# Optimization experiments

Hardware: AMD Instinct MI355X
Metric: run time of the kernel (lower is better)

Reference implementation:

```python
import jax, jax.numpy as jnp
import numpy as np

N = 50000       # node_num
E_RND = 1600000 # random edges (avg degree 32)
IN = 256        # in_dim
OUT = 128       # out_dim
NB = 10000      # queried nodes batch
SLOPE = 0.1     # leaky_relu slope_ratio


def setup_inputs() -> dict:
    key = jax.random.key(0)
    k = jax.random.split(key, 6)
    feats = jax.random.normal(k[0], (N, IN), dtype=jnp.float32)
    W = jax.random.normal(k[1], (OUT, IN), dtype=jnp.float32) * 0.05
    b = jax.random.normal(k[2], (OUT,), dtype=jnp.float32) * 0.05
    a = jax.random.normal(k[3], (2 * OUT,), dtype=jnp.float32) * 0.05
    rnd = jax.random.randint(k[4], (E_RND, 2), 0, N)
    loops = jnp.stack([jnp.arange(N), jnp.arange(N)], axis=1)  # self-loops, as in torch code
    edges = jnp.concatenate([rnd, loops], axis=0).astype(jnp.int32)  # [E,2] = (dst, src)
    node_idx = jax.random.randint(k[5], (NB,), 0, N).astype(jnp.int32)
    return dict(feats=feats, W=W, b=b, a=a, edges=edges, node_idx=node_idx)


def reference(feats, W, b, a, edges, node_idx):
    n = feats.shape[0]
    emb = feats @ W.T + b                      # [N, OUT]  (out_linear_layer)
    out_dim = emb.shape[1]
    # concat(emb[dst], emb[src]) @ a  ==  (emb @ a1)[dst] + (emb @ a2)[src]
    s_dst = emb @ a[:out_dim]                  # [N]
    s_src = emb @ a[out_dim:]                  # [N]
    dst, src = edges[:, 0], edges[:, 1]
    score = jnp.exp(jax.nn.leaky_relu(s_dst[dst] + s_src[src], negative_slope=SLOPE))  # [E]
    # sparse.mm(matrix, emb) and sparse.mm(matrix, ones) as segment sums over dst
    num = jax.ops.segment_sum(score[:, None] * emb[src], dst, num_segments=n)  # [N, OUT]
    den = jax.ops.segment_sum(score, dst, num_segments=n)                       # [N]
    out = num / den[:, None]
    return out[node_idx]
```

## Files before the change

kernel.cpp:

```cpp
#include <hip/hip_runtime.h>

#define IN_DIM 256
#define OUT_DIM 128
#define SLOPE 0.1f
#define CAP 128

typedef short bf16x8 __attribute__((ext_vector_type(8)));
typedef float f32x4  __attribute__((ext_vector_type(4)));
typedef unsigned short ushort4v __attribute__((ext_vector_type(4)));

__device__ __forceinline__ unsigned short f2bf(float f) {
    unsigned u = __builtin_bit_cast(unsigned, f);
    return (unsigned short)((u + 0x7FFFu + ((u >> 16) & 1u)) >> 16);
}

__device__ __forceinline__ void gld_lds16(const void* g, void* l) {
    __builtin_amdgcn_global_load_lds(
        (const __attribute__((address_space(1))) void*)g,
        (__attribute__((address_space(3))) void*)l, 16, 0, 0);
}

__global__ __launch_bounds__(256) void cvt_kernel(
    const float* __restrict__ feats, const float* __restrict__ W,
    unsigned short* __restrict__ fb, unsigned short* __restrict__ wb,
    int nf4, int nw4)
{
    const int stride = gridDim.x * blockDim.x;
    const int total = nf4 + nw4;
    for (int i = blockIdx.x * blockDim.x + threadIdx.x; i < total; i += stride) {
        float4 v;
        if (i < nf4) v = reinterpret_cast<const float4*>(feats)[i];
        else         v = reinterpret_cast<const float4*>(W)[i - nf4];
        ushort4v o;
        o[0] = f2bf(v.x); o[1] = f2bf(v.y); o[2] = f2bf(v.z); o[3] = f2bf(v.w);
        if (i < nf4) *reinterpret_cast<ushort4v*>(&fb[4 * (size_t)i]) = o;
        else         *reinterpret_cast<ushort4v*>(&wb[4 * (size_t)(i - nf4)]) = o;
    }
}

__global__ __launch_bounds__(256) void gemm_mfma_kernel(
    const unsigned short* __restrict__ fb, const unsigned short* __restrict__ wb,
    const float* __restrict__ bias, const float* __restrict__ a,
    unsigned short* __restrict__ emb_bf, float* __restrict__ s_dst,
    float* __restrict__ s_src, int* __restrict__ needed,
    int* __restrict__ cur, int n)
{
    __shared__ __align__(16) unsigned short A_s[128 * 128];
    __shared__ __align__(16) unsigned short W_s[128 * 128];
    __shared__ float sd_l[2][128];
    __shared__ float ss_l[2][128];

    const int t    = threadIdx.x;
    const int lane = t & 63;
    const int wid  = t >> 6;
    const int wr   = wid >> 1;
    const int wc   = wid & 1;
    const int row0 = blockIdx.x * 128;

    if (t < 128) {
        const int ci = row0 + t;
        if (ci < n) { needed[ci] = 0; cur[ci] = 0; }
    }

    const int rlo = lane >> 4;
    const int cA  = lane & 15;

    const f32x4 z4 = {0.f, 0.f, 0.f, 0.f};
    f32x4 acc[4][4];
    #pragma unroll
    for (int mi = 0; mi < 4; ++mi)
        #pragma unroll
        for (int ni = 0; ni < 4; ++ni) acc[mi][ni] = z4;

    for (int ph = 0; ph < 2; ++ph) {
        const int k0 = ph * 128;
        if (ph) __syncthreads();

        #pragma unroll
        for (int j = 0; j < 8; ++j) {
            const int slot = wid * 8 + j;
            const int r    = slot * 4 + rlo;
            const int ch   = cA ^ (r & 7);
            gld_lds16(fb + (size_t)(row0 + r) * IN_DIM + k0 + (ch << 3),
                      &A_s[slot * 512]);
            gld_lds16(wb + (size_t)r * IN_DIM + k0 + (ch << 3),
                      &W_s[slot * 512]);
        }
        __syncthreads();

        #pragma unroll
        for (int ks = 0; ks < 4; ++ks) {
            const int kf = ks * 32 + (lane >> 4) * 8;
            bf16x8 af[4], wf[4];
            #pragma unroll
            for (int mi = 0; mi < 4; ++mi) {
                const int row = wr * 64 + mi * 16 + (lane & 15);
                const int off = (row * 128 + kf) ^ ((row & 7) << 3);
                af[mi] = *(const bf16x8*)&A_s[off];
            }
            #pragma unroll
            for (int ni = 0; ni < 4; ++ni) {
                const int col = wc * 64 + ni * 16 + (lane & 15);
                const int off = (col * 128 + kf) ^ ((col & 7) << 3);
                wf[ni] = *(const bf16x8*)&W_s[off];
            }
            #pragma unroll
            for (int mi = 0; mi < 4; ++mi)
                #pragma unroll
                for (int ni = 0; ni < 4; ++ni)
                    acc[mi][ni] = __builtin_amdgcn_mfma_f32_16x16x32_bf16(
                        af[mi], wf[ni], acc[mi][ni], 0, 0, 0);
        }
    }

    float bcol[4], avd[4], avs[4];
    #pragma unroll
    for (int ni = 0; ni < 4; ++ni) {
        const int col = wc * 64 + ni * 16 + (lane & 15);
        bcol[ni] = bias[col];
        avd[ni]  = a[col];
        avs[ni]  = a[OUT_DIM + col];
    }

    #pragma unroll
    for (int mi = 0; mi < 4; ++mi) {
        #pragma unroll
        for (int j = 0; j < 4; ++j) {
            const int rib = wr * 64 + mi * 16 + (lane >> 4) * 4 + j;
            const int row = row0 + rib;
            float pd = 0.f, ps = 0.f;
            if (row < n) {
                #pragma unroll
                for (int ni = 0; ni < 4; ++ni) {
                    const float v = acc[mi][ni][j] + bcol[ni];
                    emb_bf[(size_t)row * OUT_DIM + wc * 64 + ni * 16 + (lane & 15)] = f2bf(v);
                    pd = fmaf(v, avd[ni], pd);
                    ps = fmaf(v, avs[ni], ps);
                }
            }
            pd += __shfl_xor(pd, 1); ps += __shfl_xor(ps, 1);
            pd += __shfl_xor(pd, 2); ps += __shfl_xor(ps, 2);
            pd += __shfl_xor(pd, 4); ps += __shfl_xor(ps, 4);
            pd += __shfl_xor(pd, 8); ps += __shfl_xor(ps, 8);
            if ((lane & 15) == 0) { sd_l[wc][rib] = pd; ss_l[wc][rib] = ps; }
        }
    }
    __syncthreads();
    if (t < 128) {
        const int row = row0 + t;
        if (row < n) {
            s_dst[row] = sd_l[0][t] + sd_l[1][t];
            s_src[row] = ss_l[0][t] + ss_l[1][t];
        }
    }
}

__global__ void flag_kernel(const int* __restrict__ node_idx,
                            int* __restrict__ needed, int nb)
{
    const int i = blockIdx.x * blockDim.x + threadIdx.x;
    if (i < nb) needed[node_idx[i]] = 1;
}

__global__ __launch_bounds__(256) void scatter_kernel(
    const int* __restrict__ edges, const int* __restrict__ needed,
    int* __restrict__ cur, const float* __restrict__ s_dst,
    const float* __restrict__ s_src, int2* __restrict__ ew, int E)
{
    const int e = blockIdx.x * blockDim.x + threadIdx.x;
    if (e >= E) return;
    const int2 ed = reinterpret_cast<const int2*>(edges)[e];
    if (needed[ed.x]) {
        const float x = s_dst[ed.x] + s_src[ed.y];
        const float w = __expf(x >= 0.f ? x : SLOPE * x);
        const int p = atomicAdd(&cur[ed.x], 1);
        if (p < CAP)
            ew[(size_t)ed.x * CAP + p] = make_int2(ed.y, __float_as_int(w));
    }
}

__global__ __launch_bounds__(256) void agg_out_kernel(
    const int* __restrict__ node_idx, const int* __restrict__ cur,
    const int2* __restrict__ ew, const unsigned short* __restrict__ emb_bf,
    float* __restrict__ out, int nb)
{
    const int w    = (int)((blockIdx.x * blockDim.x + threadIdx.x) >> 6);
    const int lane = threadIdx.x & 63;
    if (w >= nb) return;

    const int dst = node_idx[w];
    int m = cur[dst];
    if (m > CAP) m = CAP;
    const int2* __restrict__ bucket = ew + (size_t)dst * CAP;

    float accx = 0.f, accy = 0.f, den = 0.f;

    for (int base = 0; base < m; base += 64) {
        const int rem = min(64, m - base);
        int   src = 0;
        float wt  = 0.f;
        if (lane < rem) {
            const int2 q = bucket[base + lane];
            src = q.x;
            wt  = __int_as_float(q.y);
        }
        int i = 0;
        for (; i + 4 <= rem; i += 4) {
            const int   s0 = __shfl(src, i),     s1 = __shfl(src, i + 1);
            const int   s2 = __shfl(src, i + 2), s3 = __shfl(src, i + 3);
            const float w0 = __shfl(wt, i),      w1 = __shfl(wt, i + 1);
            const float w2 = __shfl(wt, i + 2),  w3 = __shfl(wt, i + 3);
            const unsigned b0 = *(const unsigned*)&emb_bf[(size_t)s0 * OUT_DIM + 2 * lane];
            const unsigned b1 = *(const unsigned*)&emb_bf[(size_t)s1 * OUT_DIM + 2 * lane];
            const unsigned b2 = *(const unsigned*)&emb_bf[(size_t)s2 * OUT_DIM + 2 * lane];
            const unsigned b3 = *(const unsigned*)&emb_bf[(size_t)s3 * OUT_DIM + 2 * lane];
            den += (w0 + w1) + (w2 + w3);
            accx = fmaf(w0, __int_as_float((int)(b0 << 16)), accx);
            accy = fmaf(w0, __int_as_float((int)(b0 & 0xFFFF0000u)), accy);
            accx = fmaf(w1, __int_as_float((int)(b1 << 16)), accx);
            accy = fmaf(w1, __int_as_float((int)(b1 & 0xFFFF0000u)), accy);
            accx = fmaf(w2, __int_as_float((int)(b2 << 16)), accx);
            accy = fmaf(w2, __int_as_float((int)(b2 & 0xFFFF0000u)), accy);
            accx = fmaf(w3, __int_as_float((int)(b3 << 16)), accx);
            accy = fmaf(w3, __int_as_float((int)(b3 & 0xFFFF0000u)), accy);
        }
        for (; i < rem; ++i) {
            const int   s0 = __shfl(src, i);
            const float w0 = __shfl(wt, i);
            const unsigned b0 = *(const unsigned*)&emb_bf[(size_t)s0 * OUT_DIM + 2 * lane];
            den += w0;
            accx = fmaf(w0, __int_as_float((int)(b0 << 16)), accx);
            accy = fmaf(w0, __int_as_float((int)(b0 & 0xFFFF0000u)), accy);
        }
    }

    const float inv = 1.0f / den;
    float2 o; o.x = accx * inv; o.y = accy * inv;
    *reinterpret_cast<float2*>(&out[(size_t)w * OUT_DIM + 2 * lane]) = o;
}

extern "C" void kernel_launch(void* const* d_in, const int* in_sizes, int n_in,
                              void* d_out, int out_size, void* d_ws, size_t ws_size,
                              hipStream_t stream)
{
    const float* feats    = (const float*)d_in[0];
    const float* W        = (const float*)d_in[1];
    const float* bias     = (const float*)d_in[2];
    const float* a        = (const float*)d_in[3];
    const int*   edges    = (const int*)d_in[4];
    const int*   node_idx = (const int*)d_in[5];
    float*       out      = (float*)d_out;

    const int n  = in_sizes[0] / IN_DIM;
    const int E  = in_sizes[4] / 2;
    const int nb = in_sizes[5];
    const int npad = ((n + 127) / 128) * 128;

    char* ws = (char*)d_ws;
    unsigned short* emb_bf = (unsigned short*)ws;
    ws += (size_t)n * OUT_DIM * sizeof(unsigned short);
    unsigned short* fb = (unsigned short*)ws;
    ws += (size_t)npad * IN_DIM * sizeof(unsigned short);
    unsigned short* wb = (unsigned short*)ws;
    ws += (size_t)OUT_DIM * IN_DIM * sizeof(unsigned short);
    float* s_dst = (float*)ws;  ws += (size_t)(n + 4) * sizeof(float);
    float* s_src = (float*)ws;  ws += (size_t)(n + 4) * sizeof(float);
    int*   needed= (int*)ws;    ws += (size_t)(n + 4) * sizeof(int);
    int*   cur   = (int*)ws;    ws += (size_t)(n + 4) * sizeof(int);
    int2*  ew    = (int2*)ws;   ws += (size_t)n * CAP * sizeof(int2);

    const int nf4 = n * IN_DIM / 4;
    const int nw4 = OUT_DIM * IN_DIM / 4;

    cvt_kernel      <<<2048, 256, 0, stream>>>(feats, W, fb, wb, nf4, nw4);
    gemm_mfma_kernel<<<npad / 128, 256, 0, stream>>>(
        fb, wb, bias, a, emb_bf, s_dst, s_src, needed, cur, n);
    flag_kernel     <<<(nb + 255) / 256, 256, 0, stream>>>(node_idx, needed, nb);
    scatter_kernel  <<<(E + 255) / 256, 256, 0, stream>>>(edges, needed, cur, s_dst, s_src, ew, E);
    agg_out_kernel  <<<(nb + 3) / 4, 256, 0, stream>>>(node_idx, cur, ew, emb_bf, out, nb);
}
```

Measured before the change: 69.12 us.

## Compute attention scores from fp32 feats via folded W^T a vectors before GEMM

```diff
diff --git a/kernel.cpp b/kernel.cpp
--- a/kernel.cpp
+++ b/kernel.cpp
@@ -20,55 +20,119 @@
         (__attribute__((address_space(3))) void*)l, 16, 0, 0);
 }
 
-__global__ __launch_bounds__(256) void cvt_kernel(
-    const float* __restrict__ feats, const float* __restrict__ W,
-    unsigned short* __restrict__ fb, unsigned short* __restrict__ wb,
-    int nf4, int nw4)
-{
-    const int stride = gridDim.x * blockDim.x;
-    const int total = nf4 + nw4;
-    for (int i = blockIdx.x * blockDim.x + threadIdx.x; i < total; i += stride) {
-        float4 v;
-        if (i < nf4) v = reinterpret_cast<const float4*>(feats)[i];
-        else         v = reinterpret_cast<const float4*>(W)[i - nf4];
+__global__ __launch_bounds__(256) void uv_kernel(
+    const float* __restrict__ W, const float* __restrict__ a,
+    const float* __restrict__ bias, float* __restrict__ uv)
+{
+    const int k = threadIdx.x;
+    float u = 0.f, v = 0.f;
+    for (int j = 0; j < OUT_DIM; ++j) {
+        const float w = W[(size_t)j * IN_DIM + k];
+        u = fmaf(a[j], w, u);
+        v = fmaf(a[OUT_DIM + j], w, v);
+    }
+    uv[k] = u;
+    uv[256 + k] = v;
+    if (k == 0) {
+        float cd = 0.f, cs = 0.f;
+        for (int j = 0; j < OUT_DIM; ++j) {
+            cd = fmaf(bias[j], a[j], cd);
+            cs = fmaf(bias[j], a[OUT_DIM + j], cs);
+        }
+        uv[512] = cd; uv[513] = cs;
+    }
+}
+
+__global__ __launch_bounds__(256) void cvt_score_kernel(
+    const float* __restrict__ feats, const float* __restrict__ uv,
+    unsigned short* __restrict__ fb, float* __restrict__ s_dst,
+    float* __restrict__ s_src, int* __restrict__ needed,
+    int* __restrict__ cur, int n, int npad)
+{
+    __shared__ float u_s[256], v_s[256];
+    const int t    = threadIdx.x;
+    const int lane = t & 63;
+    const int wid  = t >> 6;
+    u_s[t] = uv[t];
+    v_s[t] = uv[256 + t];
+    __syncthreads();
+
+    const int row = blockIdx.x * 4 + wid;
+    if (row >= npad) return;
+
+    if (row < n) {
+        const float4 f = *(const float4*)&feats[(size_t)row * IN_DIM + 4 * lane];
         ushort4v o;
-        o[0] = f2bf(v.x); o[1] = f2bf(v.y); o[2] = f2bf(v.z); o[3] = f2bf(v.w);
-        if (i < nf4) *reinterpret_cast<ushort4v*>(&fb[4 * (size_t)i]) = o;
-        else         *reinterpret_cast<ushort4v*>(&wb[4 * (size_t)(i - nf4)]) = o;
+        o[0] = f2bf(f.x); o[1] = f2bf(f.y); o[2] = f2bf(f.z); o[3] = f2bf(f.w);
+        *(ushort4v*)&fb[(size_t)row * IN_DIM + 4 * lane] = o;
+
+        float sd = f.x * u_s[4*lane]     + f.y * u_s[4*lane + 1]
+                 + f.z * u_s[4*lane + 2] + f.w * u_s[4*lane + 3];
+        float ss = f.x * v_s[4*lane]     + f.y * v_s[4*lane + 1]
+                 + f.z * v_s[4*lane + 2] + f.w * v_s[4*lane + 3];
+        #pragma unroll
+        for (int o2 = 32; o2 > 0; o2 >>= 1) {
+            sd += __shfl_xor(sd, o2);
+            ss += __shfl_xor(ss, o2);
+        }
+        if (lane == 0) {
+            s_dst[row] = sd + uv[512];
+            s_src[row] = ss + uv[513];
+            needed[row] = 0;
+            cur[row] = 0;
+        }
+    } else {
+        const ushort4v z = {0, 0, 0, 0};
+        *(ushort4v*)&fb[(size_t)row * IN_DIM + 4 * lane] = z;
+    }
+}
+
+__global__ void flag_kernel(const int* __restrict__ node_idx,
+                            int* __restrict__ needed, int nb)
+{
+    const int i = blockIdx.x * blockDim.x + threadIdx.x;
+    if (i < nb) needed[node_idx[i]] = 1;
+}
+
+__global__ __launch_bounds__(256) void scatter_kernel(
+    const int* __restrict__ edges, const int* __restrict__ needed,
+    int* __restrict__ cur, const float* __restrict__ s_dst,
+    const float* __restrict__ s_src, int2* __restrict__ ew, int E)
+{
+    const int e = blockIdx.x * blockDim.x + threadIdx.x;
+    if (e >= E) return;
+    const int2 ed = reinterpret_cast<const int2*>(edges)[e];
+    if (needed[ed.x]) {
+        const float x = s_dst[ed.x] + s_src[ed.y];
+        const float w = __expf(x >= 0.f ? x : SLOPE * x);
+        const int p = atomicAdd(&cur[ed.x], 1);
+        if (p < CAP)
+            ew[(size_t)ed.x * CAP + p] = make_int2(ed.y, __float_as_int(w));
     }
 }
 
 __global__ __launch_bounds__(256) void gemm_mfma_kernel(
-    const unsigned short* __restrict__ fb, const unsigned short* __restrict__ wb,
-    const float* __restrict__ bias, const float* __restrict__ a,
-    unsigned short* __restrict__ emb_bf, float* __restrict__ s_dst,
-    float* __restrict__ s_src, int* __restrict__ needed,
-    int* __restrict__ cur, int n)
-{
-    __shared__ __align__(16) unsigned short A_s[128 * 128];
+    const unsigned short* __restrict__ fb, const float* __restrict__ W,
+    const float* __restrict__ bias, unsigned short* __restrict__ emb_bf,
+    int n)
+{
+    __shared__ __align__(16) unsigned short A_s[64 * 128];
     __shared__ __align__(16) unsigned short W_s[128 * 128];
-    __shared__ float sd_l[2][128];
-    __shared__ float ss_l[2][128];
 
     const int t    = threadIdx.x;
     const int lane = t & 63;
     const int wid  = t >> 6;
     const int wr   = wid >> 1;
     const int wc   = wid & 1;
-    const int row0 = blockIdx.x * 128;
-
-    if (t < 128) {
-        const int ci = row0 + t;
-        if (ci < n) { needed[ci] = 0; cur[ci] = 0; }
-    }
+    const int row0 = blockIdx.x * 64;
 
     const int rlo = lane >> 4;
     const int cA  = lane & 15;
 
     const f32x4 z4 = {0.f, 0.f, 0.f, 0.f};
-    f32x4 acc[4][4];
+    f32x4 acc[2][4];
     #pragma unroll
-    for (int mi = 0; mi < 4; ++mi)
+    for (int mi = 0; mi < 2; ++mi)
         #pragma unroll
         for (int ni = 0; ni < 4; ++ni) acc[mi][ni] = z4;
 
@@ -77,24 +141,50 @@
         if (ph) __syncthreads();
 
         #pragma unroll
-        for (int j = 0; j < 8; ++j) {
-            const int slot = wid * 8 + j;
+        for (int j = 0; j < 4; ++j) {
+            const int slot = wid * 4 + j;
             const int r    = slot * 4 + rlo;
             const int ch   = cA ^ (r & 7);
             gld_lds16(fb + (size_t)(row0 + r) * IN_DIM + k0 + (ch << 3),
                       &A_s[slot * 512]);
-            gld_lds16(wb + (size_t)r * IN_DIM + k0 + (ch << 3),
-                      &W_s[slot * 512]);
+        }
+        #pragma unroll
+        for (int j = 0; j < 2; ++j) {
+            const int g = j * 256 + t;
+            const int r = g >> 2;
+            const int c = g & 3;
+            const float4 v0 = *(const float4*)&W[(size_t)r * IN_DIM + k0 + c * 32 + 0];
+            const float4 v1 = *(const float4*)&W[(size_t)r * IN_DIM + k0 + c * 32 + 4];
+            const float4 v2 = *(const float4*)&W[(size_t)r * IN_DIM + k0 + c * 32 + 8];
+            const float4 v3 = *(const float4*)&W[(size_t)r * IN_DIM + k0 + c * 32 + 12];
+            const float4 v4 = *(const float4*)&W[(size_t)r * IN_DIM + k0 + c * 32 + 16];
+            const float4 v5 = *(const float4*)&W[(size_t)r * IN_DIM + k0 + c * 32 + 20];
+            const float4 v6 = *(const float4*)&W[(size_t)r * IN_DIM + k0 + c * 32 + 24];
+            const float4 v7 = *(const float4*)&W[(size_t)r * IN_DIM + k0 + c * 32 + 28];
+            bf16x8 p0, p1, p2, p3;
+            p0[0]=(short)f2bf(v0.x); p0[1]=(short)f2bf(v0.y); p0[2]=(short)f2bf(v0.z); p0[3]=(short)f2bf(v0.w);
+            p0[4]=(short)f2bf(v1.x); p0[5]=(short)f2bf(v1.y); p0[6]=(short)f2bf(v1.z); p0[7]=(short)f2bf(v1.w);
+            p1[0]=(short)f2bf(v2.x); p1[1]=(short)f2bf(v2.y); p1[2]=(short)f2bf(v2.z); p1[3]=(short)f2bf(v2.w);
+            p1[4]=(short)f2bf(v3.x); p1[5]=(short)f2bf(v3.y); p1[6]=(short)f2bf(v3.z); p1[7]=(short)f2bf(v3.w);
+            p2[0]=(short)f2bf(v4.x); p2[1]=(short)f2bf(v4.y); p2[2]=(short)f2bf(v4.z); p2[3]=(short)f2bf(v4.w);
+            p2[4]=(short)f2bf(v5.x); p2[5]=(short)f2bf(v5.y); p2[6]=(short)f2bf(v5.z); p2[7]=(short)f2bf(v5.w);
+            p3[0]=(short)f2bf(v6.x); p3[1]=(short)f2bf(v6.y); p3[2]=(short)f2bf(v6.z); p3[3]=(short)f2bf(v6.w);
+            p3[4]=(short)f2bf(v7.x); p3[5]=(short)f2bf(v7.y); p3[6]=(short)f2bf(v7.z); p3[7]=(short)f2bf(v7.w);
+            const int cb = c * 4;
+            *(bf16x8*)&W_s[(r * 128) + (((cb + 0) ^ (r & 7)) << 3)] = p0;
+            *(bf16x8*)&W_s[(r * 128) + (((cb + 1) ^ (r & 7)) << 3)] = p1;
+            *(bf16x8*)&W_s[(r * 128) + (((cb + 2) ^ (r & 7)) << 3)] = p2;
+            *(bf16x8*)&W_s[(r * 128) + (((cb + 3) ^ (r & 7)) << 3)] = p3;
         }
         __syncthreads();
 
         #pragma unroll
         for (int ks = 0; ks < 4; ++ks) {
             const int kf = ks * 32 + (lane >> 4) * 8;
-            bf16x8 af[4], wf[4];
+            bf16x8 af[2], wf[4];
             #pragma unroll
-            for (int mi = 0; mi < 4; ++mi) {
-                const int row = wr * 64 + mi * 16 + (lane & 15);
+            for (int mi = 0; mi < 2; ++mi) {
+                const int row = wr * 32 + mi * 16 + (lane & 15);
                 const int off = (row * 128 + kf) ^ ((row & 7) << 3);
                 af[mi] = *(const bf16x8*)&A_s[off];
             }
@@ -105,7 +195,7 @@
                 wf[ni] = *(const bf16x8*)&W_s[off];
             }
             #pragma unroll
-            for (int mi = 0; mi < 4; ++mi)
+            for (int mi = 0; mi < 2; ++mi)
                 #pragma unroll
                 for (int ni = 0; ni < 4; ++ni)
                     acc[mi][ni] = __builtin_amdgcn_mfma_f32_16x16x32_bf16(
@@ -113,69 +203,24 @@
         }
     }
 
-    float bcol[4], avd[4], avs[4];
+    float bcol[4];
     #pragma unroll
-    for (int ni = 0; ni < 4; ++ni) {
-        const int col = wc * 64 + ni * 16 + (lane & 15);
-        bcol[ni] = bias[col];
-        avd[ni]  = a[col];
-        avs[ni]  = a[OUT_DIM + col];
-    }
+    for (int ni = 0; ni < 4; ++ni)
+        bcol[ni] = bias[wc * 64 + ni * 16 + (lane & 15)];
 
     #pragma unroll
-    for (int mi = 0; mi < 4; ++mi) {
+    for (int mi = 0; mi < 2; ++mi) {
         #pragma unroll
         for (int j = 0; j < 4; ++j) {
-            const int rib = wr * 64 + mi * 16 + (lane >> 4) * 4 + j;
-            const int row = row0 + rib;
-            float pd = 0.f, ps = 0.f;
+            const int row = row0 + wr * 32 + mi * 16 + (lane >> 4) * 4 + j;
             if (row < n) {
                 #pragma unroll
                 for (int ni = 0; ni < 4; ++ni) {
                     const float v = acc[mi][ni][j] + bcol[ni];
                     emb_bf[(size_t)row * OUT_DIM + wc * 64 + ni * 16 + (lane & 15)] = f2bf(v);
-                    pd = fmaf(v, avd[ni], pd);
-                    ps = fmaf(v, avs[ni], ps);
                 }
             }
-            pd += __shfl_xor(pd, 1); ps += __shfl_xor(ps, 1);
-            pd += __shfl_xor(pd, 2); ps += __shfl_xor(ps, 2);
-            pd += __shfl_xor(pd, 4); ps += __shfl_xor(ps, 4);
-            pd += __shfl_xor(pd, 8); ps += __shfl_xor(ps, 8);
-            if ((lane & 15) == 0) { sd_l[wc][rib] = pd; ss_l[wc][rib] = ps; }
-        }
-    }
-    __syncthreads();
-    if (t < 128) {
-        const int row = row0 + t;
-        if (row < n) {
-            s_dst[row] = sd_l[0][t] + sd_l[1][t];
-            s_src[row] = ss_l[0][t] + ss_l[1][t];
-        }
-    }
-}
-
-__global__ void flag_kernel(const int* __restrict__ node_idx,
-                            int* __restrict__ needed, int nb)
-{
-    const int i = blockIdx.x * blockDim.x + threadIdx.x;
-    if (i < nb) needed[node_idx[i]] = 1;
-}
-
-__global__ __launch_bounds__(256) void scatter_kernel(
-    const int* __restrict__ edges, const int* __restrict__ needed,
-    int* __restrict__ cur, const float* __restrict__ s_dst,
-    const float* __restrict__ s_src, int2* __restrict__ ew, int E)
-{
-    const int e = blockIdx.x * blockDim.x + threadIdx.x;
-    if (e >= E) return;
-    const int2 ed = reinterpret_cast<const int2*>(edges)[e];
-    if (needed[ed.x]) {
-        const float x = s_dst[ed.x] + s_src[ed.y];
-        const float w = __expf(x >= 0.f ? x : SLOPE * x);
-        const int p = atomicAdd(&cur[ed.x], 1);
-        if (p < CAP)
-            ew[(size_t)ed.x * CAP + p] = make_int2(ed.y, __float_as_int(w));
+        }
     }
 }
 
@@ -254,28 +299,24 @@
     const int n  = in_sizes[0] / IN_DIM;
     const int E  = in_sizes[4] / 2;
     const int nb = in_sizes[5];
-    const int npad = ((n + 127) / 128) * 128;
+    const int npad = ((n + 63) / 64) * 64;
 
     char* ws = (char*)d_ws;
     unsigned short* emb_bf = (unsigned short*)ws;
     ws += (size_t)n * OUT_DIM * sizeof(unsigned short);
     unsigned short* fb = (unsigned short*)ws;
     ws += (size_t)npad * IN_DIM * sizeof(unsigned short);
-    unsigned short* wb = (unsigned short*)ws;
-    ws += (size_t)OUT_DIM * IN_DIM * sizeof(unsigned short);
     float* s_dst = (float*)ws;  ws += (size_t)(n + 4) * sizeof(float);
     float* s_src = (float*)ws;  ws += (size_t)(n + 4) * sizeof(float);
     int*   needed= (int*)ws;    ws += (size_t)(n + 4) * sizeof(int);
     int*   cur   = (int*)ws;    ws += (size_t)(n + 4) * sizeof(int);
+    float* uv    = (float*)ws;  ws += 516 * sizeof(float);
     int2*  ew    = (int2*)ws;   ws += (size_t)n * CAP * sizeof(int2);
 
-    const int nf4 = n * IN_DIM / 4;
-    const int nw4 = OUT_DIM * IN_DIM / 4;
-
-    cvt_kernel      <<<2048, 256, 0, stream>>>(feats, W, fb, wb, nf4, nw4);
-    gemm_mfma_kernel<<<npad / 128, 256, 0, stream>>>(
-        fb, wb, bias, a, emb_bf, s_dst, s_src, needed, cur, n);
+    uv_kernel       <<<1, 256, 0, stream>>>(W, a, bias, uv);
+    cvt_score_kernel<<<npad / 4, 256, 0, stream>>>(feats, uv, fb, s_dst, s_src, needed, cur, n, npad);
     flag_kernel     <<<(nb + 255) / 256, 256, 0, stream>>>(node_idx, needed, nb);
     scatter_kernel  <<<(E + 255) / 256, 256, 0, stream>>>(edges, needed, cur, s_dst, s_src, ew, E);
+    gemm_mfma_kernel<<<npad / 64, 256, 0, stream>>>(fb, W, bias, emb_bf, n);
     agg_out_kernel  <<<(nb + 3) / 4, 256, 0, stream>>>(node_idx, cur, ew, emb_bf, out, nb);
 }
```

Result: slower. 91.99 us (+33.1%).
